# Kernel optimization log

Measured on AMD Instinct MI355X. Metric: run time of the kernel, lower is better.

## Reference

```python
import jax, jax.numpy as jnp
import numpy as np

N = 60000   # nodes per siamese side
E = 960000  # edges per side (avg degree 16)
B = 32      # graphs per batch
F = 38      # input node features
H = 128     # h_ch == out_ch
EPS = 1e-5


def graph_conv(x, edge_index, W_rel, W_root, b):
    # PyG GraphConv (aggr='add'): lin_rel(sum_j x_j) + lin_root(x_i) + bias
    src, dst = edge_index[0], edge_index[1]
    agg = jax.ops.segment_sum(x[src], dst, num_segments=x.shape[0])
    return agg @ W_rel + x @ W_root + b


def batch_norm(x, gamma, beta):
    # training-mode BN over the node dimension (biased variance)
    mu = x.mean(axis=0)
    var = x.var(axis=0)
    return (x - mu) * jax.lax.rsqrt(var + EPS) * gamma + beta


def embed(x, edge_index, batch,
          W1r, W1s, b1, g1, be1,
          W2r, W2s, b2, g2, be2,
          W3r, W3s, b3, g3, be3,
          Wg1, bg1, Wg2, bg2):
    h1 = jax.nn.relu(batch_norm(graph_conv(x, edge_index, W1r, W1s, b1), g1, be1))
    h2 = jax.nn.relu(batch_norm(graph_conv(h1, edge_index, W2r, W2s, b2), g2, be2))
    ho = jax.nn.relu(batch_norm(graph_conv(h2, edge_index, W3r, W3s, b3), g3, be3))
    # GlobalAttentionSelect, pool_ref='last': gate from last conv output
    gate = jax.nn.relu(jax.nn.relu(ho @ Wg1 + bg1) @ Wg2 + bg2)  # [N,1]
    gmax = jax.ops.segment_max(gate, batch, num_segments=B)       # [B,1]
    eg = jnp.exp(gate - gmax[batch])
    denom = jax.ops.segment_sum(eg, batch, num_segments=B)
    attn = eg / denom[batch]                                      # per-graph softmax
    return jax.ops.segment_sum(attn * ho, batch, num_segments=B)  # [B,H]


def setup_inputs() -> dict:
    key = jax.random.key(0)
    ks = jax.random.split(key, 40)
    s = 0.05
    inp = {
        "x1": jax.random.normal(ks[0], (N, F), dtype=jnp.float32),
        "x2": jax.random.normal(ks[1], (N, F), dtype=jnp.float32),
        "edge_index1": jax.random.randint(ks[2], (2, E), 0, N),
        "edge_index2": jax.random.randint(ks[3], (2, E), 0, N),
        "batch1": jnp.sort(jax.random.randint(ks[4], (N,), 0, B)),
        "batch2": jnp.sort(jax.random.randint(ks[5], (N,), 0, B)),
        # conv1: F->H
        "W1r": jax.random.normal(ks[6], (F, H), dtype=jnp.float32) * s,
        "W1s": jax.random.normal(ks[7], (F, H), dtype=jnp.float32) * s,
        "b1": jnp.zeros((H,), jnp.float32),
        "g1": jnp.ones((H,), jnp.float32), "be1": jnp.zeros((H,), jnp.float32),
        # conv2: H->H
        "W2r": jax.random.normal(ks[8], (H, H), dtype=jnp.float32) * s,
        "W2s": jax.random.normal(ks[9], (H, H), dtype=jnp.float32) * s,
        "b2": jnp.zeros((H,), jnp.float32),
        "g2": jnp.ones((H,), jnp.float32), "be2": jnp.zeros((H,), jnp.float32),
        # conv_out: H->H
        "W3r": jax.random.normal(ks[10], (H, H), dtype=jnp.float32) * s,
        "W3s": jax.random.normal(ks[11], (H, H), dtype=jnp.float32) * s,
        "b3": jnp.zeros((H,), jnp.float32),
        "g3": jnp.ones((H,), jnp.float32), "be3": jnp.zeros((H,), jnp.float32),
        # gate MLP: H->32->1 (final ReLU)
        "Wg1": jax.random.normal(ks[12], (H, 32), dtype=jnp.float32) * s,
        "bg1": jnp.zeros((32,), jnp.float32),
        "Wg2": jax.random.normal(ks[13], (32, 1), dtype=jnp.float32) * s,
        "bg2": jnp.zeros((1,), jnp.float32),
        # final MLP on |e1-e2|: H->64->1
        "Wf1": jax.random.normal(ks[14], (H, 64), dtype=jnp.float32) * s,
        "bf1": jnp.zeros((64,), jnp.float32),
        "Wf2": jax.random.normal(ks[15], (64, 1), dtype=jnp.float32) * s,
        "bf2": jnp.zeros((1,), jnp.float32),
    }
    return inp


def reference(x1, x2, edge_index1, edge_index2, batch1, batch2,
              W1r, W1s, b1, g1, be1,
              W2r, W2s, b2, g2, be2,
              W3r, W3s, b3, g3, be3,
              Wg1, bg1, Wg2, bg2,
              Wf1, bf1, Wf2, bf2):
    e1 = embed(x1, edge_index1, batch1, W1r, W1s, b1, g1, be1,
               W2r, W2s, b2, g2, be2, W3r, W3s, b3, g3, be3,
               Wg1, bg1, Wg2, bg2)
    e2 = embed(x2, edge_index2, batch2, W1r, W1s, b1, g1, be1,
               W2r, W2s, b2, g2, be2, W3r, W3s, b3, g3, be3,
               Wg1, bg1, Wg2, bg2)
    d = jnp.abs(e1 - e2)                       # final_out_join='abs'
    out = jax.nn.relu(d @ Wf1 + bf1) @ Wf2 + bf2  # [B,1]
    return out
```

## Files before the change

kernel.cpp:

```cpp
#include <hip/hip_runtime.h>
#include <cstdint>
#include <cstddef>

#define NN 60000
#define NE 960000
#define NB 32
#define FIN 38
#define HH 128
#define SCB 235

typedef short bf16x8 __attribute__((ext_vector_type(8)));
typedef float f32x4 __attribute__((ext_vector_type(4)));

__device__ __forceinline__ unsigned short f2bf(float x) {
  unsigned u = __builtin_bit_cast(unsigned, x);
  u = u + 0x7fffu + ((u >> 16) & 1u);
  return (unsigned short)(u >> 16);
}
__device__ __forceinline__ float bf2f(unsigned short h) {
  unsigned u = ((unsigned)h) << 16;
  return __builtin_bit_cast(float, u);
}

__global__ __launch_bounds__(256) void k_hist(const int* __restrict__ ei0,
                                              const int* __restrict__ ei1,
                                              int* __restrict__ counts) {
  int s = blockIdx.y;
  const int* ei = s ? ei1 : ei0;
  int i = blockIdx.x * 256 + threadIdx.x;
  if (i < NE) atomicAdd(&counts[s * NN + ei[NE + i]], 1);
}

__global__ __launch_bounds__(256) void k_scan1(const int* __restrict__ counts_,
                                               int* __restrict__ rowptr_,
                                               int* __restrict__ bsum) {
  int s = blockIdx.y, b = blockIdx.x, t = threadIdx.x;
  int idx = b * 256 + t;
  const int* counts = counts_ + (size_t)s * NN;
  int* rowptr = rowptr_ + (size_t)s * (NN + 1);
  __shared__ int sm[256];
  int c = (idx < NN) ? counts[idx] : 0;
  sm[t] = c;
  __syncthreads();
  for (int off = 1; off < 256; off <<= 1) {
    int v = (t >= off) ? sm[t - off] : 0;
    __syncthreads();
    sm[t] += v;
    __syncthreads();
  }
  if (idx < NN) rowptr[idx] = sm[t] - c;
  if (t == 255) bsum[s * SCB + b] = sm[255];
}

__global__ __launch_bounds__(256) void k_scan2(const int* __restrict__ bsum,
                                               int* __restrict__ boff,
                                               int* __restrict__ rowptr_) {
  int s = blockIdx.x, t = threadIdx.x;
  __shared__ int sm[256];
  int v = (t < SCB) ? bsum[s * SCB + t] : 0;
  sm[t] = v;
  __syncthreads();
  for (int off = 1; off < 256; off <<= 1) {
    int u = (t >= off) ? sm[t - off] : 0;
    __syncthreads();
    sm[t] += u;
    __syncthreads();
  }
  if (t < SCB) boff[s * SCB + t] = sm[t] - v;
  if (t == 255) rowptr_[(size_t)s * (NN + 1) + NN] = sm[255];
}

__global__ __launch_bounds__(256) void k_scan3(int* __restrict__ rowptr_,
                                               int* __restrict__ cursor_,
                                               const int* __restrict__ boff) {
  int s = blockIdx.y, b = blockIdx.x, t = threadIdx.x;
  int idx = b * 256 + t;
  if (idx < NN) {
    int v = rowptr_[(size_t)s * (NN + 1) + idx] + boff[s * SCB + b];
    rowptr_[(size_t)s * (NN + 1) + idx] = v;
    cursor_[(size_t)s * NN + idx] = v;
  }
}

__global__ __launch_bounds__(256) void k_scatter(const int* __restrict__ ei0,
                                                 const int* __restrict__ ei1,
                                                 int* __restrict__ cursor,
                                                 unsigned short* __restrict__ col) {
  int s = blockIdx.y;
  const int* ei = s ? ei1 : ei0;
  int i = blockIdx.x * 256 + threadIdx.x;
  if (i < NE) {
    int dst = ei[NE + i];
    int src = ei[i];
    int pos = atomicAdd(&cursor[s * NN + dst], 1);
    col[(size_t)s * NE + pos] = (unsigned short)src;
  }
}

template <int W>
__global__ __launch_bounds__(256) void k_agg(const float* __restrict__ h0,
                                             const float* __restrict__ h1,
                                             const int* __restrict__ rowptr_,
                                             const unsigned short* __restrict__ col_,
                                             float* __restrict__ agg_) {
  int s = blockIdx.y;
  const float* h = s ? h1 : h0;
  const int* rowptr = rowptr_ + (size_t)s * (NN + 1);
  const unsigned short* col = col_ + (size_t)s * NE;
  float* agg = agg_ + (size_t)s * NN * W;
  int wave = threadIdx.x >> 6;
  int lane = threadIdx.x & 63;
  int node = blockIdx.x * 4 + wave;
  if (node >= NN) return;
  int s0 = rowptr[node], s1 = rowptr[node + 1];
  if (W == 128) {
    float2 acc = make_float2(0.f, 0.f);
    const float* hp = h + (lane << 1);
    int j = s0;
    for (; j + 3 < s1; j += 4) {
      int a0 = col[j], a1 = col[j + 1], a2 = col[j + 2], a3 = col[j + 3];
      float2 v0 = *reinterpret_cast<const float2*>(hp + (size_t)a0 * 128);
      float2 v1 = *reinterpret_cast<const float2*>(hp + (size_t)a1 * 128);
      float2 v2 = *reinterpret_cast<const float2*>(hp + (size_t)a2 * 128);
      float2 v3 = *reinterpret_cast<const float2*>(hp + (size_t)a3 * 128);
      acc.x += (v0.x + v1.x) + (v2.x + v3.x);
      acc.y += (v0.y + v1.y) + (v2.y + v3.y);
    }
    for (; j < s1; ++j) {
      int a0 = col[j];
      float2 v0 = *reinterpret_cast<const float2*>(hp + (size_t)a0 * 128);
      acc.x += v0.x;
      acc.y += v0.y;
    }
    *reinterpret_cast<float2*>(agg + (size_t)node * 128 + (lane << 1)) = acc;
  } else {
    float2 acc = make_float2(0.f, 0.f);
    if (lane < 19) {
      const float* hp = h + (lane << 1);
      int j = s0;
      for (; j + 1 < s1; j += 2) {
        int a0 = col[j], a1 = col[j + 1];
        float2 v0 = *reinterpret_cast<const float2*>(hp + (size_t)a0 * W);
        float2 v1 = *reinterpret_cast<const float2*>(hp + (size_t)a1 * W);
        acc.x += v0.x + v1.x;
        acc.y += v0.y + v1.y;
      }
      if (j < s1) {
        float2 v = *reinterpret_cast<const float2*>(hp + (size_t)col[j] * W);
        acc.x += v.x;
        acc.y += v.y;
      }
      *reinterpret_cast<float2*>(agg + (size_t)node * W + (lane << 1)) = acc;
    }
  }
}

template <bool VEC>
__global__ __launch_bounds__(256) void k_gemm_mfma(
    const float* __restrict__ A_, int lda, const float* __restrict__ X0,
    const float* __restrict__ X1, int ldx, const float* __restrict__ Wr,
    const float* __restrict__ Ws, const float* __restrict__ bias, int K,
    float* __restrict__ Z_, float* __restrict__ stats_) {
  int side = blockIdx.y;
  const float* A = A_ + (size_t)side * NN * lda;
  const float* X = side ? X1 : X0;
  float* Z = Z_ + (size_t)side * NN * HH;
  float* stats = stats_ + (size_t)side * 256;

  __shared__ __align__(16) unsigned char sAh[64 * 64];
  __shared__ __align__(16) unsigned char sAl[64 * 64];
  __shared__ __align__(16) unsigned char sXh[64 * 64];
  __shared__ __align__(16) unsigned char sXl[64 * 64];
  __shared__ __align__(16) unsigned char sBh[2][128 * 64];
  __shared__ __align__(16) unsigned char sBl[2][128 * 64];

  int t = threadIdx.x;
  int l = t & 63;
  int wid = t >> 6;
  int wr = wid >> 1, wc = wid & 1;
  int row0 = blockIdx.x * 64;

  f32x4 acc[2][4];
#pragma unroll
  for (int rt = 0; rt < 2; ++rt)
#pragma unroll
    for (int ct = 0; ct < 4; ++ct) acc[rt][ct] = (f32x4)(0.f);

  int nK = (K + 31) >> 5;
  for (int ks = 0; ks < nK; ++ks) {
    {
      int r = t >> 2;
      int kc = (t & 3) << 3;
      int grow = row0 + r;
      float av[8], xv[8];
      if (VEC) {
        float4 a0 = make_float4(0, 0, 0, 0), a1 = a0, x0 = a0, x1 = a0;
        if (grow < NN) {
          const float* pa = A + (size_t)grow * lda + (ks << 5) + kc;
          const float* px = X + (size_t)grow * ldx + (ks << 5) + kc;
          a0 = *reinterpret_cast<const float4*>(pa);
          a1 = *reinterpret_cast<const float4*>(pa + 4);
          x0 = *reinterpret_cast<const float4*>(px);
          x1 = *reinterpret_cast<const float4*>(px + 4);
        }
        av[0] = a0.x; av[1] = a0.y; av[2] = a0.z; av[3] = a0.w;
        av[4] = a1.x; av[5] = a1.y; av[6] = a1.z; av[7] = a1.w;
        xv[0] = x0.x; xv[1] = x0.y; xv[2] = x0.z; xv[3] = x0.w;
        xv[4] = x1.x; xv[5] = x1.y; xv[6] = x1.z; xv[7] = x1.w;
      } else {
#pragma unroll
        for (int e = 0; e < 8; ++e) {
          int gk = (ks << 5) + kc + e;
          bool ok = (grow < NN) && (gk < K);
          av[e] = ok ? A[(size_t)grow * lda + gk] : 0.f;
          xv[e] = ok ? X[(size_t)grow * ldx + gk] : 0.f;
        }
      }
      bf16x8 ah, al, xh, xl;
#pragma unroll
      for (int e = 0; e < 8; ++e) {
        unsigned short h = f2bf(av[e]);
        ah[e] = (short)h;
        al[e] = (short)f2bf(av[e] - bf2f(h));
        h = f2bf(xv[e]);
        xh[e] = (short)h;
        xl[e] = (short)f2bf(xv[e] - bf2f(h));
      }
      int off = ((r << 6) + (kc << 1)) ^ ((r & 7) << 4);
      *reinterpret_cast<bf16x8*>(sAh + off) = ah;
      *reinterpret_cast<bf16x8*>(sAl + off) = al;
      *reinterpret_cast<bf16x8*>(sXh + off) = xh;
      *reinterpret_cast<bf16x8*>(sXl + off) = xl;
    }
    {
      int kq = t >> 5;
      int c0 = (t & 31) << 2;
      float wf[2][4][4];
#pragma unroll
      for (int kk = 0; kk < 4; ++kk) {
        int gk = (ks << 5) + (kq << 2) + kk;
        float4 vr = make_float4(0, 0, 0, 0), vs = vr;
        if (gk < K) {
          vr = *reinterpret_cast<const float4*>(Wr + (size_t)gk * HH + c0);
          vs = *reinterpret_cast<const float4*>(Ws + (size_t)gk * HH + c0);
        }
        wf[0][kk][0] = vr.x; wf[0][kk][1] = vr.y; wf[0][kk][2] = vr.z; wf[0][kk][3] = vr.w;
        wf[1][kk][0] = vs.x; wf[1][kk][1] = vs.y; wf[1][kk][2] = vs.z; wf[1][kk][3] = vs.w;
      }
#pragma unroll
      for (int m = 0; m < 2; ++m) {
#pragma unroll
        for (int j = 0; j < 4; ++j) {
          int c = c0 + j;
          unsigned h0 = f2bf(wf[m][0][j]), h1 = f2bf(wf[m][1][j]);
          unsigned h2 = f2bf(wf[m][2][j]), h3 = f2bf(wf[m][3][j]);
          unsigned l0 = f2bf(wf[m][0][j] - bf2f((unsigned short)h0));
          unsigned l1 = f2bf(wf[m][1][j] - bf2f((unsigned short)h1));
          unsigned l2 = f2bf(wf[m][2][j] - bf2f((unsigned short)h2));
          unsigned l3 = f2bf(wf[m][3][j] - bf2f((unsigned short)h3));
          uint2 hv = make_uint2(h0 | (h1 << 16), h2 | (h3 << 16));
          uint2 lv = make_uint2(l0 | (l1 << 16), l2 | (l3 << 16));
          int off = ((c << 6) + (kq << 3)) ^ ((c & 7) << 4);
          *reinterpret_cast<uint2*>(sBh[m] + off) = hv;
          *reinterpret_cast<uint2*>(sBl[m] + off) = lv;
        }
      }
    }
    __syncthreads();
    bf16x8 fah[2], fal[2], fxh[2], fxl[2];
    int ko = (l >> 4) << 4;
#pragma unroll
    for (int rt = 0; rt < 2; ++rt) {
      int rr = (wr << 5) + (rt << 4) + (l & 15);
      int off = ((rr << 6) + ko) ^ ((rr & 7) << 4);
      fah[rt] = *reinterpret_cast<const bf16x8*>(sAh + off);
      fal[rt] = *reinterpret_cast<const bf16x8*>(sAl + off);
      fxh[rt] = *reinterpret_cast<const bf16x8*>(sXh + off);
      fxl[rt] = *reinterpret_cast<const bf16x8*>(sXl + off);
    }
#pragma unroll
    for (int ct = 0; ct < 4; ++ct) {
      int cc = (wc << 6) + (ct << 4) + (l & 15);
      int off = ((cc << 6) + ko) ^ ((cc & 7) << 4);
      bf16x8 brh = *reinterpret_cast<const bf16x8*>(sBh[0] + off);
      bf16x8 brl = *reinterpret_cast<const bf16x8*>(sBl[0] + off);
      bf16x8 bsh = *reinterpret_cast<const bf16x8*>(sBh[1] + off);
      bf16x8 bsl = *reinterpret_cast<const bf16x8*>(sBl[1] + off);
#pragma unroll
      for (int rt = 0; rt < 2; ++rt) {
        f32x4 c = acc[rt][ct];
        c = __builtin_amdgcn_mfma_f32_16x16x32_bf16(fah[rt], brh, c, 0, 0, 0);
        c = __builtin_amdgcn_mfma_f32_16x16x32_bf16(fah[rt], brl, c, 0, 0, 0);
        c = __builtin_amdgcn_mfma_f32_16x16x32_bf16(fal[rt], brh, c, 0, 0, 0);
        c = __builtin_amdgcn_mfma_f32_16x16x32_bf16(fxh[rt], bsh, c, 0, 0, 0);
        c = __builtin_amdgcn_mfma_f32_16x16x32_bf16(fxh[rt], bsl, c, 0, 0, 0);
        c = __builtin_amdgcn_mfma_f32_16x16x32_bf16(fxl[rt], bsh, c, 0, 0, 0);
        acc[rt][ct] = c;
      }
    }
    __syncthreads();
  }

  float ps[4] = {0, 0, 0, 0}, pq[4] = {0, 0, 0, 0};
#pragma unroll
  for (int ct = 0; ct < 4; ++ct) {
    int col = (wc << 6) + (ct << 4) + (l & 15);
    float b = bias[col];
#pragma unroll
    for (int rt = 0; rt < 2; ++rt) {
      int rbase = row0 + (wr << 5) + (rt << 4) + ((l >> 4) << 2);
      f32x4 v = acc[rt][ct];
#pragma unroll
      for (int rg = 0; rg < 4; ++rg) {
        int row = rbase + rg;
        if (row < NN) {
          float z = v[rg] + b;
          Z[(size_t)row * HH + col] = z;
          ps[ct] += z;
          pq[ct] += z * z;
        }
      }
    }
  }
#pragma unroll
  for (int ct = 0; ct < 4; ++ct) {
    ps[ct] += __shfl_xor(ps[ct], 16, 64);
    ps[ct] += __shfl_xor(ps[ct], 32, 64);
    pq[ct] += __shfl_xor(pq[ct], 16, 64);
    pq[ct] += __shfl_xor(pq[ct], 32, 64);
  }
  if (l < 16) {
#pragma unroll
    for (int ct = 0; ct < 4; ++ct) {
      int col = (wc << 6) + (ct << 4) + l;
      atomicAdd(&stats[col], ps[ct]);
      atomicAdd(&stats[HH + col], pq[ct]);
    }
  }
}

__global__ void k_bnfin(const float* __restrict__ stats_, const float* __restrict__ g,
                        const float* __restrict__ be, float* __restrict__ ss_) {
  int s = blockIdx.x;
  const float* stats = stats_ + (size_t)s * 256;
  float* ss = ss_ + (size_t)s * 256;
  int c = threadIdx.x;
  if (c < HH) {
    float mu = stats[c] * (1.0f / NN);
    float var = stats[HH + c] * (1.0f / NN) - mu * mu;
    float inv = 1.0f / sqrtf(var + 1e-5f);
    float sc = g[c] * inv;
    ss[c] = sc;
    ss[HH + c] = be[c] - mu * sc;
  }
}

__global__ __launch_bounds__(256) void k_bnrelu(float* __restrict__ ZH_,
                                                const float* __restrict__ ss_) {
  int s = blockIdx.y;
  float* ZH = ZH_ + (size_t)s * NN * HH;
  const float* ss = ss_ + (size_t)s * 256;
  size_t i = (size_t)blockIdx.x * 256 + threadIdx.x;
  float4 z = *reinterpret_cast<float4*>(ZH + i * 4);
  int c = (int)((i * 4) & 127);
  float4 sc = *reinterpret_cast<const float4*>(ss + c);
  float4 sh = *reinterpret_cast<const float4*>(ss + HH + c);
  z.x = fmaxf(z.x * sc.x + sh.x, 0.f);
  z.y = fmaxf(z.y * sc.y + sh.y, 0.f);
  z.z = fmaxf(z.z * sc.z + sh.z, 0.f);
  z.w = fmaxf(z.w * sc.w + sh.w, 0.f);
  *reinterpret_cast<float4*>(ZH + i * 4) = z;
}

__global__ __launch_bounds__(256) void k_gate(const float* __restrict__ Ho_,
                                              const float* __restrict__ Wg1,
                                              const float* __restrict__ bg1,
                                              const float* __restrict__ Wg2,
                                              const float* __restrict__ bg2,
                                              float* __restrict__ gate_) {
  int s = blockIdx.y;
  const float* Ho = Ho_ + (size_t)s * NN * HH;
  float* gate = gate_ + (size_t)s * NN;
  __shared__ float sW[128 * 32];
  int t = threadIdx.x;
  for (int i = t; i < 128 * 32 / 4; i += 256)
    *reinterpret_cast<float4*>(&sW[i * 4]) =
        *reinterpret_cast<const float4*>(Wg1 + i * 4);
  __syncthreads();
  int lane = t & 63, wv = t >> 6;
  int half = lane >> 5, l = lane & 31;
  float w2 = Wg2[l];
  float b2 = bg2[0];
  float b1v = bg1[l];
  for (int it = 0; it < 16; ++it) {
    int node = blockIdx.x * 128 + it * 8 + wv * 2 + half;
    if (node < NN) {
      const float* hr = Ho + (size_t)node * 128;
      float acc = b1v;
      for (int k = 0; k < 128; k += 4) {
        float4 hv = *reinterpret_cast<const float4*>(hr + k);
        acc += hv.x * sW[(k) * 32 + l];
        acc += hv.y * sW[(k + 1) * 32 + l];
        acc += hv.z * sW[(k + 2) * 32 + l];
        acc += hv.w * sW[(k + 3) * 32 + l];
      }
      float v = fmaxf(acc, 0.f) * w2;
#pragma unroll
      for (int off = 16; off > 0; off >>= 1) v += __shfl_down(v, off, 32);
      if (l == 0) gate[node] = fmaxf(v + b2, 0.f);
    }
  }
}

__global__ void k_bounds(const int* __restrict__ batch0,
                         const int* __restrict__ batch1,
                         int* __restrict__ starts, int* __restrict__ ends) {
  int s = blockIdx.x;
  const int* batch = s ? batch1 : batch0;
  int g = threadIdx.x;
  if (g >= NB) return;
  int lo = 0, hi = NN;
  while (lo < hi) { int mid = (lo + hi) >> 1; if (batch[mid] < g) lo = mid + 1; else hi = mid; }
  starts[s * NB + g] = lo;
  lo = 0; hi = NN;
  while (lo < hi) { int mid = (lo + hi) >> 1; if (batch[mid] < g + 1) lo = mid + 1; else hi = mid; }
  ends[s * NB + g] = lo;
}

__global__ __launch_bounds__(256) void k_gstat(const float* __restrict__ gate_,
                                               const int* __restrict__ starts,
                                               const int* __restrict__ ends,
                                               float* __restrict__ gm,
                                               float* __restrict__ dn) {
  int sd = blockIdx.y;
  int b = blockIdx.x;
  const float* gate = gate_ + (size_t)sd * NN;
  __shared__ float red[256];
  int t = threadIdx.x;
  int s = starts[sd * NB + b], en = ends[sd * NB + b];
  float m = -3.402823e38f;
  for (int i = s + t; i < en; i += 256) m = fmaxf(m, gate[i]);
  red[t] = m;
  __syncthreads();
  for (int off = 128; off > 0; off >>= 1) {
    if (t < off) red[t] = fmaxf(red[t], red[t + off]);
    __syncthreads();
  }
  float gmax = red[0];
  __syncthreads();
  float ds = 0;
  for (int i = s + t; i < en; i += 256) ds += expf(gate[i] - gmax);
  red[t] = ds;
  __syncthreads();
  for (int off = 128; off > 0; off >>= 1) {
    if (t < off) red[t] += red[t + off];
    __syncthreads();
  }
  if (t == 0) {
    gm[sd * NB + b] = gmax;
    dn[sd * NB + b] = red[0];
  }
}

#define SPL 8
__global__ __launch_bounds__(256) void k_poolsum(const float* __restrict__ Ho_,
                                                 const float* __restrict__ gate_,
                                                 const int* __restrict__ starts,
                                                 const int* __restrict__ ends,
                                                 const float* __restrict__ gm,
                                                 const float* __restrict__ dn,
                                                 float* __restrict__ e) {
  int sd = blockIdx.y;
  int b = blockIdx.x;
  int z = blockIdx.z;
  const float* Ho = Ho_ + (size_t)sd * NN * HH;
  const float* gate = gate_ + (size_t)sd * NN;
  __shared__ float red[256];
  int t = threadIdx.x;
  int s = starts[sd * NB + b], en = ends[sd * NB + b];
  int len = en - s;
  if (len <= 0) return;
  int chunk = (len + SPL - 1) / SPL;
  int i0 = s + z * chunk;
  int i1 = min(en, i0 + chunk);
  if (i0 >= i1) return;
  float gmax = gm[sd * NB + b];
  float invdn = 1.0f / dn[sd * NB + b];
  int c = t & 127, half = t >> 7;
  float acc = 0;
  for (int i = i0 + half; i < i1; i += 2)
    acc += expf(gate[i] - gmax) * Ho[(size_t)i * 128 + c];
  red[t] = acc;
  __syncthreads();
  if (t < 128)
    atomicAdd(&e[(size_t)sd * NB * HH + (size_t)b * HH + t],
              (red[t] + red[t + 128]) * invdn);
}

__global__ void k_final(const float* __restrict__ e, const float* __restrict__ Wf1,
                        const float* __restrict__ bf1, const float* __restrict__ Wf2,
                        const float* __restrict__ bf2, float* __restrict__ out) {
  int b = blockIdx.x, j = threadIdx.x;
  float acc = bf1[j];
  const float* e1 = e + (size_t)b * 128;
  const float* e2 = e + (size_t)NB * 128 + (size_t)b * 128;
  for (int k = 0; k < 128; ++k) {
    float d = fabsf(e1[k] - e2[k]);
    acc += d * Wf1[k * 64 + j];
  }
  float v = fmaxf(acc, 0.f) * Wf2[j];
#pragma unroll
  for (int off = 32; off > 0; off >>= 1) v += __shfl_down(v, off, 64);
  if (j == 0) out[b] = v + bf2[0];
}

extern "C" void kernel_launch(void* const* d_in, const int* in_sizes, int n_in,
                              void* d_out, int out_size, void* d_ws, size_t ws_size,
                              hipStream_t stream) {
  const float* x0 = (const float*)d_in[0];
  const float* x1 = (const float*)d_in[1];
  const int* ei0 = (const int*)d_in[2];
  const int* ei1 = (const int*)d_in[3];
  const int* batch0 = (const int*)d_in[4];
  const int* batch1 = (const int*)d_in[5];
  const float* W1r = (const float*)d_in[6];
  const float* W1s = (const float*)d_in[7];
  const float* b1 = (const float*)d_in[8];
  const float* g1 = (const float*)d_in[9];
  const float* be1 = (const float*)d_in[10];
  const float* W2r = (const float*)d_in[11];
  const float* W2s = (const float*)d_in[12];
  const float* b2 = (const float*)d_in[13];
  const float* g2 = (const float*)d_in[14];
  const float* be2 = (const float*)d_in[15];
  const float* W3r = (const float*)d_in[16];
  const float* W3s = (const float*)d_in[17];
  const float* b3 = (const float*)d_in[18];
  const float* g3 = (const float*)d_in[19];
  const float* be3 = (const float*)d_in[20];
  const float* Wg1 = (const float*)d_in[21];
  const float* bg1 = (const float*)d_in[22];
  const float* Wg2 = (const float*)d_in[23];
  const float* bg2 = (const float*)d_in[24];
  const float* Wf1 = (const float*)d_in[25];
  const float* bf1 = (const float*)d_in[26];
  const float* Wf2 = (const float*)d_in[27];
  const float* bf2 = (const float*)d_in[28];

  char* p = (char*)d_ws;
  auto alloc = [&](size_t bytes) {
    void* r = (void*)p;
    p += (bytes + 255) & ~(size_t)255;
    return r;
  };
  int* counts = (int*)alloc((size_t)2 * NN * 4);
  int* rowptr = (int*)alloc((size_t)2 * (NN + 1) * 4);
  int* cursor = (int*)alloc((size_t)2 * NN * 4);
  unsigned short* col = (unsigned short*)alloc((size_t)2 * NE * 2);
  int* bsum = (int*)alloc(2 * SCB * 4);
  int* boff = (int*)alloc(2 * SCB * 4);
  int* starts = (int*)alloc(2 * NB * 4);
  int* ends = (int*)alloc(2 * NB * 4);
  float* stats = (float*)alloc(2 * 256 * 4);
  float* ss = (float*)alloc(2 * 256 * 4);
  float* gate = (float*)alloc((size_t)2 * NN * 4);
  float* gm = (float*)alloc(2 * NB * 4);
  float* dn = (float*)alloc(2 * NB * 4);
  float* ebuf = (float*)alloc((size_t)2 * NB * HH * 4);
  float* bufA = (float*)alloc((size_t)2 * NN * HH * 4);
  float* bufB = (float*)alloc((size_t)2 * NN * HH * 4);
  float* bufC = (float*)alloc((size_t)2 * NN * HH * 4);

  hipMemsetAsync(counts, 0, (size_t)2 * NN * 4, stream);
  k_hist<<<dim3((NE + 255) / 256, 2), 256, 0, stream>>>(ei0, ei1, counts);
  k_scan1<<<dim3(SCB, 2), 256, 0, stream>>>(counts, rowptr, bsum);
  k_scan2<<<2, 256, 0, stream>>>(bsum, boff, rowptr);
  k_scan3<<<dim3(SCB, 2), 256, 0, stream>>>(rowptr, cursor, boff);
  k_scatter<<<dim3((NE + 255) / 256, 2), 256, 0, stream>>>(ei0, ei1, cursor, col);

  k_agg<38><<<dim3(15000, 2), 256, 0, stream>>>(x0, x1, rowptr, col, bufA);
  hipMemsetAsync(stats, 0, 2 * 256 * 4, stream);
  k_gemm_mfma<false><<<dim3(938, 2), 256, 0, stream>>>(
      bufA, FIN, x0, x1, FIN, W1r, W1s, b1, FIN, bufB, stats);
  k_bnfin<<<2, 128, 0, stream>>>(stats, g1, be1, ss);
  k_bnrelu<<<dim3(7500, 2), 256, 0, stream>>>(bufB, ss);

  k_agg<128><<<dim3(15000, 2), 256, 0, stream>>>(bufB, bufB + (size_t)NN * HH,
                                                 rowptr, col, bufA);
  hipMemsetAsync(stats, 0, 2 * 256 * 4, stream);
  k_gemm_mfma<true><<<dim3(938, 2), 256, 0, stream>>>(
      bufA, HH, bufB, bufB + (size_t)NN * HH, HH, W2r, W2s, b2, HH, bufC, stats);
  k_bnfin<<<2, 128, 0, stream>>>(stats, g2, be2, ss);
  k_bnrelu<<<dim3(7500, 2), 256, 0, stream>>>(bufC, ss);

  k_agg<128><<<dim3(15000, 2), 256, 0, stream>>>(bufC, bufC + (size_t)NN * HH,
                                                 rowptr, col, bufA);
  hipMemsetAsync(stats, 0, 2 * 256 * 4, stream);
  k_gemm_mfma<true><<<dim3(938, 2), 256, 0, stream>>>(
      bufA, HH, bufC, bufC + (size_t)NN * HH, HH, W3r, W3s, b3, HH, bufB, stats);
  k_bnfin<<<2, 128, 0, stream>>>(stats, g3, be3, ss);
  k_bnrelu<<<dim3(7500, 2), 256, 0, stream>>>(bufB, ss);

  k_gate<<<dim3(469, 2), 256, 0, stream>>>(bufB, Wg1, bg1, Wg2, bg2, gate);
  k_bounds<<<2, 32, 0, stream>>>(batch0, batch1, starts, ends);
  hipMemsetAsync(ebuf, 0, (size_t)2 * NB * HH * 4, stream);
  k_gstat<<<dim3(NB, 2), 256, 0, stream>>>(gate, starts, ends, gm, dn);
  k_poolsum<<<dim3(NB, 2, SPL), 256, 0, stream>>>(bufB, gate, starts, ends, gm, dn,
                                                  ebuf);

  k_final<<<NB, 64, 0, stream>>>(ebuf, Wf1, bf1, Wf2, bf2, (float*)d_out);
}
```

Measured before the change: 1.261 ms.

## Precompute bf16 split weight images and double GEMM row tile with 512 threads

A new prep kernel converts each layer's W_rel/W_root into swizzled hi/lo bf16 shared-memory images once. Each GEMM block then copies the prepared image straight into LDS instead of loading fp32 weights and splitting them again in every block. Blocks grow to 512 threads covering 128 rows, which halves the number of blocks and the number of weight staging passes. The cost is larger LDS use per block, which may lower occupancy, plus three small extra kernel launches.

```diff
diff --git a/kernel.cpp b/kernel.cpp
--- a/kernel.cpp
+++ b/kernel.cpp
@@ -155,30 +155,69 @@
   }
 }
 
+__global__ __launch_bounds__(256) void k_wprep(const float* __restrict__ Wr,
+                                               const float* __restrict__ Ws,
+                                               int K, unsigned char* __restrict__ img) {
+  int ks = blockIdx.x;
+  int t = threadIdx.x;
+  unsigned char* dst = img + (size_t)ks * 32768;
+  int kq = t >> 5;
+  int c0 = (t & 31) << 2;
+  float wf[2][4][4];
+#pragma unroll
+  for (int kk = 0; kk < 4; ++kk) {
+    int gk = (ks << 5) + (kq << 2) + kk;
+    float4 vr = make_float4(0, 0, 0, 0), vs = vr;
+    if (gk < K) {
+      vr = *reinterpret_cast<const float4*>(Wr + (size_t)gk * HH + c0);
+      vs = *reinterpret_cast<const float4*>(Ws + (size_t)gk * HH + c0);
+    }
+    wf[0][kk][0] = vr.x; wf[0][kk][1] = vr.y; wf[0][kk][2] = vr.z; wf[0][kk][3] = vr.w;
+    wf[1][kk][0] = vs.x; wf[1][kk][1] = vs.y; wf[1][kk][2] = vs.z; wf[1][kk][3] = vs.w;
+  }
+#pragma unroll
+  for (int m = 0; m < 2; ++m) {
+#pragma unroll
+    for (int j = 0; j < 4; ++j) {
+      int c = c0 + j;
+      unsigned h0 = f2bf(wf[m][0][j]), h1 = f2bf(wf[m][1][j]);
+      unsigned h2 = f2bf(wf[m][2][j]), h3 = f2bf(wf[m][3][j]);
+      unsigned l0 = f2bf(wf[m][0][j] - bf2f((unsigned short)h0));
+      unsigned l1 = f2bf(wf[m][1][j] - bf2f((unsigned short)h1));
+      unsigned l2 = f2bf(wf[m][2][j] - bf2f((unsigned short)h2));
+      unsigned l3 = f2bf(wf[m][3][j] - bf2f((unsigned short)h3));
+      uint2 hv = make_uint2(h0 | (h1 << 16), h2 | (h3 << 16));
+      uint2 lv = make_uint2(l0 | (l1 << 16), l2 | (l3 << 16));
+      int off = ((c << 6) + (kq << 3)) ^ ((c & 7) << 4);
+      *reinterpret_cast<uint2*>(dst + m * 8192 + off) = hv;
+      *reinterpret_cast<uint2*>(dst + 16384 + m * 8192 + off) = lv;
+    }
+  }
+}
+
 template <bool VEC>
-__global__ __launch_bounds__(256) void k_gemm_mfma(
+__global__ __launch_bounds__(512) void k_gemm_mfma(
     const float* __restrict__ A_, int lda, const float* __restrict__ X0,
-    const float* __restrict__ X1, int ldx, const float* __restrict__ Wr,
-    const float* __restrict__ Ws, const float* __restrict__ bias, int K,
-    float* __restrict__ Z_, float* __restrict__ stats_) {
+    const float* __restrict__ X1, int ldx, const unsigned char* __restrict__ wimg,
+    const float* __restrict__ bias, int K, float* __restrict__ Z_,
+    float* __restrict__ stats_) {
   int side = blockIdx.y;
   const float* A = A_ + (size_t)side * NN * lda;
   const float* X = side ? X1 : X0;
   float* Z = Z_ + (size_t)side * NN * HH;
   float* stats = stats_ + (size_t)side * 256;
 
-  __shared__ __align__(16) unsigned char sAh[64 * 64];
-  __shared__ __align__(16) unsigned char sAl[64 * 64];
-  __shared__ __align__(16) unsigned char sXh[64 * 64];
-  __shared__ __align__(16) unsigned char sXl[64 * 64];
-  __shared__ __align__(16) unsigned char sBh[2][128 * 64];
-  __shared__ __align__(16) unsigned char sBl[2][128 * 64];
+  __shared__ __align__(16) unsigned char sAh[128 * 64];
+  __shared__ __align__(16) unsigned char sAl[128 * 64];
+  __shared__ __align__(16) unsigned char sXh[128 * 64];
+  __shared__ __align__(16) unsigned char sXl[128 * 64];
+  __shared__ __align__(16) unsigned char sW[4 * 8192];
 
   int t = threadIdx.x;
   int l = t & 63;
   int wid = t >> 6;
   int wr = wid >> 1, wc = wid & 1;
-  int row0 = blockIdx.x * 64;
+  int row0 = blockIdx.x * 128;
 
   f32x4 acc[2][4];
 #pragma unroll
@@ -233,37 +272,12 @@
       *reinterpret_cast<bf16x8*>(sXl + off) = xl;
     }
     {
-      int kq = t >> 5;
-      int c0 = (t & 31) << 2;
-      float wf[2][4][4];
-#pragma unroll
-      for (int kk = 0; kk < 4; ++kk) {
-        int gk = (ks << 5) + (kq << 2) + kk;
-        float4 vr = make_float4(0, 0, 0, 0), vs = vr;
-        if (gk < K) {
-          vr = *reinterpret_cast<const float4*>(Wr + (size_t)gk * HH + c0);
-          vs = *reinterpret_cast<const float4*>(Ws + (size_t)gk * HH + c0);
-        }
-        wf[0][kk][0] = vr.x; wf[0][kk][1] = vr.y; wf[0][kk][2] = vr.z; wf[0][kk][3] = vr.w;
-        wf[1][kk][0] = vs.x; wf[1][kk][1] = vs.y; wf[1][kk][2] = vs.z; wf[1][kk][3] = vs.w;
-      }
-#pragma unroll
-      for (int m = 0; m < 2; ++m) {
-#pragma unroll
-        for (int j = 0; j < 4; ++j) {
-          int c = c0 + j;
-          unsigned h0 = f2bf(wf[m][0][j]), h1 = f2bf(wf[m][1][j]);
-          unsigned h2 = f2bf(wf[m][2][j]), h3 = f2bf(wf[m][3][j]);
-          unsigned l0 = f2bf(wf[m][0][j] - bf2f((unsigned short)h0));
-          unsigned l1 = f2bf(wf[m][1][j] - bf2f((unsigned short)h1));
-          unsigned l2 = f2bf(wf[m][2][j] - bf2f((unsigned short)h2));
-          unsigned l3 = f2bf(wf[m][3][j] - bf2f((unsigned short)h3));
-          uint2 hv = make_uint2(h0 | (h1 << 16), h2 | (h3 << 16));
-          uint2 lv = make_uint2(l0 | (l1 << 16), l2 | (l3 << 16));
-          int off = ((c << 6) + (kq << 3)) ^ ((c & 7) << 4);
-          *reinterpret_cast<uint2*>(sBh[m] + off) = hv;
-          *reinterpret_cast<uint2*>(sBl[m] + off) = lv;
-        }
+      const uint4* src = reinterpret_cast<const uint4*>(wimg + (size_t)ks * 32768);
+      uint4* dst = reinterpret_cast<uint4*>(sW);
+#pragma unroll
+      for (int i = 0; i < 4; ++i) {
+        int idx = t + i * 512;
+        dst[idx] = src[idx];
       }
     }
     __syncthreads();
@@ -282,10 +296,10 @@
     for (int ct = 0; ct < 4; ++ct) {
       int cc = (wc << 6) + (ct << 4) + (l & 15);
       int off = ((cc << 6) + ko) ^ ((cc & 7) << 4);
-      bf16x8 brh = *reinterpret_cast<const bf16x8*>(sBh[0] + off);
-      bf16x8 brl = *reinterpret_cast<const bf16x8*>(sBl[0] + off);
-      bf16x8 bsh = *reinterpret_cast<const bf16x8*>(sBh[1] + off);
-      bf16x8 bsl = *reinterpret_cast<const bf16x8*>(sBl[1] + off);
+      bf16x8 brh = *reinterpret_cast<const bf16x8*>(sW + off);
+      bf16x8 bsh = *reinterpret_cast<const bf16x8*>(sW + 8192 + off);
+      bf16x8 brl = *reinterpret_cast<const bf16x8*>(sW + 16384 + off);
+      bf16x8 bsl = *reinterpret_cast<const bf16x8*>(sW + 24576 + off);
 #pragma unroll
       for (int rt = 0; rt < 2; ++rt) {
         f32x4 c = acc[rt][ct];
@@ -567,9 +581,16 @@
   float* gm = (float*)alloc(2 * NB * 4);
   float* dn = (float*)alloc(2 * NB * 4);
   float* ebuf = (float*)alloc((size_t)2 * NB * HH * 4);
+  unsigned char* wimg1 = (unsigned char*)alloc(2 * 32768);
+  unsigned char* wimg2 = (unsigned char*)alloc(4 * 32768);
+  unsigned char* wimg3 = (unsigned char*)alloc(4 * 32768);
   float* bufA = (float*)alloc((size_t)2 * NN * HH * 4);
   float* bufB = (float*)alloc((size_t)2 * NN * HH * 4);
   float* bufC = (float*)alloc((size_t)2 * NN * HH * 4);
+
+  k_wprep<<<2, 256, 0, stream>>>(W1r, W1s, FIN, wimg1);
+  k_wprep<<<4, 256, 0, stream>>>(W2r, W2s, HH, wimg2);
+  k_wprep<<<4, 256, 0, stream>>>(W3r, W3s, HH, wimg3);
 
   hipMemsetAsync(counts, 0, (size_t)2 * NN * 4, stream);
   k_hist<<<dim3((NE + 255) / 256, 2), 256, 0, stream>>>(ei0, ei1, counts);
@@ -580,24 +601,24 @@
 
   k_agg<38><<<dim3(15000, 2), 256, 0, stream>>>(x0, x1, rowptr, col, bufA);
   hipMemsetAsync(stats, 0, 2 * 256 * 4, stream);
-  k_gemm_mfma<false><<<dim3(938, 2), 256, 0, stream>>>(
-      bufA, FIN, x0, x1, FIN, W1r, W1s, b1, FIN, bufB, stats);
+  k_gemm_mfma<false><<<dim3(469, 2), 512, 0, stream>>>(
+      bufA, FIN, x0, x1, FIN, wimg1, b1, FIN, bufB, stats);
   k_bnfin<<<2, 128, 0, stream>>>(stats, g1, be1, ss);
   k_bnrelu<<<dim3(7500, 2), 256, 0, stream>>>(bufB, ss);
 
   k_agg<128><<<dim3(15000, 2), 256, 0, stream>>>(bufB, bufB + (size_t)NN * HH,
                                                  rowptr, col, bufA);
   hipMemsetAsync(stats, 0, 2 * 256 * 4, stream);
-  k_gemm_mfma<true><<<dim3(938, 2), 256, 0, stream>>>(
-      bufA, HH, bufB, bufB + (size_t)NN * HH, HH, W2r, W2s, b2, HH, bufC, stats);
+  k_gemm_mfma<true><<<dim3(469, 2), 512, 0, stream>>>(
+      bufA, HH, bufB, bufB + (size_t)NN * HH, HH, wimg2, b2, HH, bufC, stats);
   k_bnfin<<<2, 128, 0, stream>>>(stats, g2, be2, ss);
   k_bnrelu<<<dim3(7500, 2), 256, 0, stream>>>(bufC, ss);
 
   k_agg<128><<<dim3(15000, 2), 256, 0, stream>>>(bufC, bufC + (size_t)NN * HH,
                                                  rowptr, col, bufA);
   hipMemsetAsync(stats, 0, 2 * 256 * 4, stream);
-  k_gemm_mfma<true><<<dim3(938, 2), 256, 0, stream>>>(
-      bufA, HH, bufC, bufC + (size_t)NN * HH, HH, W3r, W3s, b3, HH, bufB, stats);
+  k_gemm_mfma<true><<<dim3(469, 2), 512, 0, stream>>>(
+      bufA, HH, bufC, bufC + (size_t)NN * HH, HH, wimg3, b3, HH, bufB, stats);
   k_bnfin<<<2, 128, 0, stream>>>(stats, g3, be3, ss);
   k_bnrelu<<<dim3(7500, 2), 256, 0, stream>>>(bufB, ss);
 
```

Measured after the change: 1.209 ms. 1.04x faster.
